# Kernel optimization log

Measured on AMD Instinct MI355X. Metric: run time of the kernel, lower is better.

The kernel has to match this reference:

```python
import jax, jax.numpy as jnp
import numpy as np

N = 50000
E = 800000
D = 128


def setup_inputs() -> dict:
    key = jax.random.key(0)
    ks = jax.random.split(key, 10)
    x = jax.random.normal(ks[0], (N, D), dtype=jnp.float32)
    edge_index = jax.random.randint(ks[1], (2, E), 0, N, dtype=jnp.int32)
    s = 1.0 / np.sqrt(D)
    W1 = jax.random.uniform(ks[2], (D, D), jnp.float32, -s, s)
    b1 = jnp.zeros((D,), jnp.float32)
    W2 = jax.random.uniform(ks[3], (D, D), jnp.float32, -s, s)
    b2 = jnp.zeros((D,), jnp.float32)
    Wt = jax.random.uniform(ks[4], (D, 1), jnp.float32, -s, s)
    bt = jnp.zeros((1,), jnp.float32)
    We = jax.random.uniform(ks[5], (D, 1), jnp.float32, -s, s)
    be = jnp.zeros((1,), jnp.float32)
    return {"x": x, "edge_index": edge_index, "W1": W1, "b1": b1,
            "W2": W2, "b2": b2, "Wt": Wt, "bt": bt, "We": We, "be": be}


def _gcn_norm(edge_index, n):
    # add self-loops, then symmetric normalization D^-1/2 (A+I) D^-1/2
    loop = jnp.arange(n, dtype=edge_index.dtype)
    src = jnp.concatenate([edge_index[0], loop])
    dst = jnp.concatenate([edge_index[1], loop])
    ones = jnp.ones(src.shape[0], dtype=jnp.float32)
    deg = jax.ops.segment_sum(ones, dst, num_segments=n)
    dinv = jnp.where(deg > 0, jax.lax.rsqrt(deg), 0.0)
    norm = dinv[src] * dinv[dst]  # [E+N]
    return src, dst, norm


def _gcn_conv(h, W, b, src, dst, norm, n):
    h = h @ W                                   # [N, D'] dense GEMM
    msg = h[src] * norm[:, None]                # gather + scale
    out = jax.ops.segment_sum(msg, dst, num_segments=n)  # scatter-add
    return out + b


def reference(x, edge_index, W1, b1, W2, b2, Wt, bt, We, be):
    n = x.shape[0]
    src, dst, norm = _gcn_norm(edge_index, n)
    h = jax.nn.relu(_gcn_conv(x, W1, b1, src, dst, norm, n))
    h = jax.nn.relu(_gcn_conv(h, W2, b2, src, dst, norm, n))
    # dropout is identity at inference (eval mode)
    survival_time = h @ Wt + bt   # [N, 1]
    event_status = h @ We + be    # [N, 1]
    return survival_time, event_status
```

## Files before the change

### kernel.cpp

```cpp
#include <hip/hip_runtime.h>
#include <hip/hip_fp16.h>
#include <math.h>

#define NN 50000
#define NE 800000
#define DD 128

#define NB  196
#define CAP 5300
#define EPB 4096

#define CONV_B 6250

#define SLAB (NN * 32)

typedef _Float16 half8_t __attribute__((ext_vector_type(8)));
typedef float f32x4 __attribute__((ext_vector_type(4)));


__global__ __launch_bounds__(256) void k_init_bcur(int* __restrict__ bcur) {
    int t = threadIdx.x;
    if (t < NB) bcur[t] = t * CAP;
}

__global__ __launch_bounds__(256) void k_phaseA(const int* __restrict__ src, const int* __restrict__ dst,
                                                int* __restrict__ bcur, unsigned int* __restrict__ ebuf) {
    __shared__ int hist[256];
    __shared__ int scanbuf[256];
    __shared__ int gbase[256];
    __shared__ unsigned int stage[EPB];
    __shared__ int tgt[EPB];

    const int tid = threadIdx.x;
    const int e0  = blockIdx.x * EPB;
    int nE = NE - e0; if (nE > EPB) nE = EPB;

    hist[tid] = 0;
    __syncthreads();

    unsigned int pk[16];
    unsigned int br[16];
    #pragma unroll
    for (int j = 0; j < 16; ++j) {
        int idx = tid + j * 256;
        if (idx < nE) {
            int e = e0 + idx;
            int s = src[e], d = dst[e];
            int b = d >> 8;
            int r = atomicAdd(&hist[b], 1);
            pk[j] = (unsigned int)s | ((unsigned int)(d & 255) << 16);
            br[j] = (unsigned int)b | ((unsigned int)r << 8);
        }
    }
    __syncthreads();
    int v = hist[tid];
    scanbuf[tid] = v;
    __syncthreads();
    for (int o = 1; o < 256; o <<= 1) {
        int t2 = (tid >= o) ? scanbuf[tid - o] : 0;
        __syncthreads();
        scanbuf[tid] += t2;
        __syncthreads();
    }
    int base_excl = scanbuf[tid] - v;
    if (tid < NB && v > 0) gbase[tid] = atomicAdd(&bcur[tid], v);
    hist[tid] = base_excl;
    __syncthreads();

    #pragma unroll
    for (int j = 0; j < 16; ++j) {
        int idx = tid + j * 256;
        if (idx < nE) {
            int b = br[j] & 255;
            int r = (int)(br[j] >> 8);
            int pos = hist[b] + r;
            stage[pos] = pk[j];
            tgt[pos]   = gbase[b] + r;
        }
    }
    __syncthreads();
    #pragma unroll
    for (int j = 0; j < 16; ++j) {
        int idx = tid + j * 256;
        if (idx < nE) ebuf[tgt[idx]] = stage[idx];
    }
}

__global__ __launch_bounds__(256) void k_build_csr(const unsigned int* __restrict__ ebuf,
                                                   const int* __restrict__ bcur,
                                                   int* __restrict__ row_ptr,
                                                   float* __restrict__ dinv,
                                                   unsigned short* __restrict__ col) {
    __shared__ int cnt[256];
    __shared__ int scanb[256];
    __shared__ unsigned short stage[CAP];

    const int b   = blockIdx.x;
    const int tid = threadIdx.x;
    const int seg0 = b * CAP;
    const int sb   = bcur[b] - seg0;
    const int n0   = b << 8;
    int nb = NN - n0; if (nb > 256) nb = 256;

    int sz_t = (tid < NB) ? (bcur[tid] - tid * CAP) : 0;
    scanb[tid] = sz_t;
    __syncthreads();
    for (int o = 1; o < 256; o <<= 1) {
        int t = (tid >= o) ? scanb[tid - o] : 0;
        __syncthreads();
        scanb[tid] += t;
        __syncthreads();
    }
    const int rbase = scanb[b] - sb;
    __syncthreads();

    cnt[tid] = 0;
    __syncthreads();
    for (int p = tid; p < sb; p += 256) {
        unsigned int e = ebuf[seg0 + p];
        atomicAdd(&cnt[(e >> 16) & 255], 1);
    }
    __syncthreads();
    int v = cnt[tid];
    scanb[tid] = v;
    __syncthreads();
    for (int o = 1; o < 256; o <<= 1) {
        int t = (tid >= o) ? scanb[tid - o] : 0;
        __syncthreads();
        scanb[tid] += t;
        __syncthreads();
    }
    int excl = scanb[tid] - v;
    if (tid < nb) {
        row_ptr[n0 + tid] = rbase + excl;
        dinv[n0 + tid] = rsqrtf(1.0f + (float)v);
    }
    if (b == 0 && tid == 0) row_ptr[NN] = NE;
    cnt[tid] = excl;
    __syncthreads();
    for (int p = tid; p < sb; p += 256) {
        unsigned int e = ebuf[seg0 + p];
        int pos = atomicAdd(&cnt[(e >> 16) & 255], 1);
        stage[pos] = (unsigned short)(e & 0xFFFFu);
    }
    __syncthreads();
    for (int p = tid; p < sb; p += 256) {
        col[rbase + p] = stage[p];
    }
}


__global__ __launch_bounds__(256) void k_prep(const float* __restrict__ x,
                                              const float* __restrict__ W1, const float* __restrict__ W2,
                                              __half* __restrict__ Xh,
                                              __half* __restrict__ WT1, __half* __restrict__ WT2) {
    int b = blockIdx.x;
    int tid = threadIdx.x;
    if (b < CONV_B) {
        int idx = b * 256 + tid;
        if (idx < (NN * DD) / 4) {
            float4 v = ((const float4*)x)[idx];
            __half2 a = __floats2half2_rn(v.x, v.y);
            __half2 c = __floats2half2_rn(v.z, v.w);
            uint2 pk;
            pk.x = *(unsigned int*)&a;
            pk.y = *(unsigned int*)&c;
            int row = idx >> 5;
            int c16 = idx & 31;
            int ch = c16 >> 3, wi = c16 & 7;
            *(uint2*)(Xh + (size_t)ch * SLAB + (size_t)row * 32 + wi * 4) = pk;
        }
    } else {
        const float* W  = (b == CONV_B) ? W1 : W2;
        __half*      WT = (b == CONV_B) ? WT1 : WT2;
        int n = tid >> 1;
        int k0 = (tid & 1) * 64;
        #pragma unroll 8
        for (int j = 0; j < 64; ++j) {
            int k = k0 + j;
            WT[n * DD + k] = __float2half(W[k * DD + n]);
        }
    }
}


#define LPAD 136

__global__ __launch_bounds__(256) void k_gemm_mfma(const __half* __restrict__ Xc, const __half* __restrict__ WT,
                                                   const float* __restrict__ dinv, __half* __restrict__ Gc) {
    __shared__ __half Wl[DD * LPAD];
    __shared__ __half Al[64 * LPAD];

    const int tid  = threadIdx.x;
    const int row0 = blockIdx.x * 64;

    {
        const uint4* WTg = (const uint4*)WT;
        #pragma unroll
        for (int j = 0; j < 8; ++j) {
            int u = tid + j * 256;
            int n = u >> 4, koff = (u & 15) * 8;
            uint4 v = WTg[u];
            *(uint4*)&Wl[n * LPAD + koff] = v;
        }
    }
    {
        #pragma unroll
        for (int j = 0; j < 4; ++j) {
            int u = tid + j * 256;
            int r = u >> 4, c16 = u & 15;
            int ch = c16 >> 2, wi = c16 & 3;
            int grow = row0 + r;
            uint4 v;
            if (grow < NN) v = *(const uint4*)(Xc + (size_t)ch * SLAB + (size_t)grow * 32 + wi * 8);
            else { v.x = 0; v.y = 0; v.z = 0; v.w = 0; }
            *(uint4*)&Al[r * LPAD + c16 * 8] = v;
        }
    }
    __syncthreads();

    const int wave = tid >> 6;
    const int lane = tid & 63;
    const int m    = lane & 15;
    const int quad = lane >> 4;

    f32x4 acc[8];
    #pragma unroll
    for (int t = 0; t < 8; ++t) acc[t] = (f32x4){0.f, 0.f, 0.f, 0.f};

    #pragma unroll
    for (int kk = 0; kk < DD; kk += 32) {
        half8_t a = *(const half8_t*)&Al[(wave * 16 + m) * LPAD + kk + quad * 8];
        #pragma unroll
        for (int t = 0; t < 8; ++t) {
            half8_t b = *(const half8_t*)&Wl[(t * 16 + m) * LPAD + kk + quad * 8];
            acc[t] = __builtin_amdgcn_mfma_f32_16x16x32_f16(a, b, acc[t], 0, 0, 0);
        }
    }

    __syncthreads();

    float4 dv = *(const float4*)&dinv[row0 + wave * 16 + quad * 4];

    #pragma unroll
    for (int t = 0; t < 8; ++t) {
        #pragma unroll
        for (int r = 0; r < 4; ++r) {
            int row_l = wave * 16 + quad * 4 + r;
            int c     = t * 16 + m;
            float val = acc[t][r] * ((const float*)&dv)[r];
            Al[row_l * LPAD + c] = __float2half(val);
        }
    }
    __syncthreads();

    {
        #pragma unroll
        for (int j = 0; j < 4; ++j) {
            int u = tid + j * 256;
            int r = u >> 4, c16 = u & 15;
            int ch = c16 >> 2, wi = c16 & 3;
            int grow = row0 + r;
            if (grow < NN) {
                uint4 v = *(const uint4*)&Al[r * LPAD + c16 * 8];
                *(uint4*)(Gc + (size_t)ch * SLAB + (size_t)grow * 32 + wi * 8) = v;
            }
        }
    }
}


__device__ inline float4 h4_to_f4(uint2 r) {
    __half2 a = *(__half2*)&r.x;
    __half2 b = *(__half2*)&r.y;
    float2 lo = __half22float2(a), hi = __half22float2(b);
    return make_float4(lo.x, lo.y, hi.x, hi.y);
}

__device__ inline uint2 f4_to_h4(float4 v) {
    __half2 a = __floats2half2_rn(v.x, v.y);
    __half2 b = __floats2half2_rn(v.z, v.w);
    uint2 r;
    r.x = *(unsigned int*)&a;
    r.y = *(unsigned int*)&b;
    return r;
}

__device__ inline float4 gather_grp(const __half* __restrict__ slab, int node, int fq,
                                    const unsigned short* __restrict__ col, int beg, int end) {
    float4 accA = h4_to_f4(*(const uint2*)(slab + (size_t)node * 32 + fq * 4));
    float4 accB = make_float4(0.f, 0.f, 0.f, 0.f);
    int p = beg;
    for (; p + 3 < end; p += 4) {
        int s0 = col[p], s1 = col[p + 1], s2 = col[p + 2], s3 = col[p + 3];
        float4 v0 = h4_to_f4(*(const uint2*)(slab + (size_t)s0 * 32 + fq * 4));
        float4 v1 = h4_to_f4(*(const uint2*)(slab + (size_t)s1 * 32 + fq * 4));
        float4 v2 = h4_to_f4(*(const uint2*)(slab + (size_t)s2 * 32 + fq * 4));
        float4 v3 = h4_to_f4(*(const uint2*)(slab + (size_t)s3 * 32 + fq * 4));
        accA.x += v0.x + v1.x; accA.y += v0.y + v1.y; accA.z += v0.z + v1.z; accA.w += v0.w + v1.w;
        accB.x += v2.x + v3.x; accB.y += v2.y + v3.y; accB.z += v2.z + v3.z; accB.w += v2.w + v3.w;
    }
    for (; p < end; ++p) {
        int s0 = col[p];
        float4 v0 = h4_to_f4(*(const uint2*)(slab + (size_t)s0 * 32 + fq * 4));
        accA.x += v0.x; accA.y += v0.y; accA.z += v0.z; accA.w += v0.w;
    }
    accA.x += accB.x; accA.y += accB.y; accA.z += accB.z; accA.w += accB.w;
    return accA;
}

__global__ __launch_bounds__(256) void k_aggregate_c(const __half* __restrict__ G, const float* __restrict__ dinv,
                                                     const int* __restrict__ row_ptr, const unsigned short* __restrict__ col,
                                                     const float* __restrict__ bias, __half* __restrict__ H) {
    const int bx    = blockIdx.x;
    const int slot  = bx & 7;
    const int chunk = slot >> 1;
    const int nb    = (bx >> 3) * 2 + (slot & 1);
    const int g     = threadIdx.x >> 3;
    const int fq    = threadIdx.x & 7;
    const int node  = nb * 32 + g;
    if (node >= NN) return;

    const __half* slab = G + (size_t)chunk * SLAB;
    int beg = row_ptr[node];
    int end = row_ptr[node + 1];
    float4 acc = gather_grp(slab, node, fq, col, beg, end);

    float di = dinv[node];
    float4 bv = *(const float4*)(bias + chunk * 32 + fq * 4);
    float4 hv;
    hv.x = fmaxf(fmaf(di, acc.x, bv.x), 0.f);
    hv.y = fmaxf(fmaf(di, acc.y, bv.y), 0.f);
    hv.z = fmaxf(fmaf(di, acc.z, bv.z), 0.f);
    hv.w = fmaxf(fmaf(di, acc.w, bv.w), 0.f);
    *(uint2*)(H + (size_t)chunk * SLAB + (size_t)node * 32 + fq * 4) = f4_to_h4(hv);
}

__global__ __launch_bounds__(256) void k_aggregate_heads_c(const __half* __restrict__ G, const float* __restrict__ dinv,
                                                           const int* __restrict__ row_ptr, const unsigned short* __restrict__ col,
                                                           const float* __restrict__ bias,
                                                           const float* __restrict__ Wt, const float* __restrict__ bt,
                                                           const float* __restrict__ We, const float* __restrict__ be,
                                                           float* __restrict__ out) {
    const int bx    = blockIdx.x;
    const int slot  = bx & 7;
    const int chunk = slot >> 1;
    const int nb    = (bx >> 3) * 2 + (slot & 1);
    const int g     = threadIdx.x >> 3;
    const int fq    = threadIdx.x & 7;
    const int node  = nb * 32 + g;
    if (node >= NN) return;

    const __half* slab = G + (size_t)chunk * SLAB;
    int beg = row_ptr[node];
    int end = row_ptr[node + 1];
    float4 acc = gather_grp(slab, node, fq, col, beg, end);

    float di = dinv[node];
    float4 bv = *(const float4*)(bias + chunk * 32 + fq * 4);
    float hx = fmaxf(fmaf(di, acc.x, bv.x), 0.f);
    float hy = fmaxf(fmaf(di, acc.y, bv.y), 0.f);
    float hz = fmaxf(fmaf(di, acc.z, bv.z), 0.f);
    float hw = fmaxf(fmaf(di, acc.w, bv.w), 0.f);

    float4 wt = *(const float4*)(Wt + chunk * 32 + fq * 4);
    float4 we = *(const float4*)(We + chunk * 32 + fq * 4);
    float t  = hx * wt.x + hy * wt.y + hz * wt.z + hw * wt.w;
    float ev = hx * we.x + hy * we.y + hz * we.z + hw * we.w;
    #pragma unroll
    for (int o = 1; o < 8; o <<= 1) {
        t  += __shfl_xor(t, o, 64);
        ev += __shfl_xor(ev, o, 64);
    }
    if (fq == 0) {
        if (chunk == 0) { t += bt[0]; ev += be[0]; }
        atomicAdd(&out[node], t);
        atomicAdd(&out[NN + node], ev);
    }
}


extern "C" void kernel_launch(void* const* d_in, const int* in_sizes, int n_in,
                              void* d_out, int out_size, void* d_ws, size_t ws_size,
                              hipStream_t stream) {
    const float* x  = (const float*)d_in[0];
    const int*   ei = (const int*)d_in[1];
    const float* W1 = (const float*)d_in[2];
    const float* b1 = (const float*)d_in[3];
    const float* W2 = (const float*)d_in[4];
    const float* b2 = (const float*)d_in[5];
    const float* Wt = (const float*)d_in[6];
    const float* bt = (const float*)d_in[7];
    const float* We = (const float*)d_in[8];
    const float* be = (const float*)d_in[9];
    float* out = (float*)d_out;

    const int* srcI = ei;
    const int* dstI = ei + NE;

    char* w = (char*)d_ws;
    __half*         Xh    = (__half*)w;         w += (size_t)NN * DD * sizeof(__half);
    __half*         Gh    = (__half*)w;         w += (size_t)NN * DD * sizeof(__half);
    __half*         H1h   = (__half*)w;         w += (size_t)NN * DD * sizeof(__half);
    __half*         WT1   = (__half*)w;         w += (size_t)DD * DD * sizeof(__half);
    __half*         WT2   = (__half*)w;         w += (size_t)DD * DD * sizeof(__half);
    unsigned int*   ebuf  = (unsigned int*)w;   w += (size_t)NB * CAP * sizeof(unsigned int);
    unsigned short* col   = (unsigned short*)w; w += (size_t)NE * sizeof(unsigned short);
    float*          dinv  = (float*)w;          w += (size_t)(NN + 64) * sizeof(float);
    int*            rowp  = (int*)w;            w += (size_t)(NN + 1) * sizeof(int);
    int*            bcur  = (int*)w;            w += (size_t)NB * sizeof(int);

    const int A_B    = (NE + EPB - 1) / EPB;
    const int NBLK   = (NN + 31) / 32;
    const int AGG_B  = ((NBLK + 1) / 2) * 8;
    const int GEMM_B = (NN + 63) / 64;

    hipMemsetAsync(out, 0, (size_t)out_size * sizeof(float), stream);

    hipLaunchKernelGGL(k_init_bcur,  dim3(1),          dim3(256), 0, stream, bcur);
    hipLaunchKernelGGL(k_phaseA,     dim3(A_B),        dim3(256), 0, stream, srcI, dstI, bcur, ebuf);
    hipLaunchKernelGGL(k_build_csr,  dim3(NB),         dim3(256), 0, stream, ebuf, bcur, rowp, dinv, col);
    hipLaunchKernelGGL(k_prep,       dim3(CONV_B + 2), dim3(256), 0, stream, x, W1, W2, Xh, WT1, WT2);

    hipLaunchKernelGGL(k_gemm_mfma,   dim3(GEMM_B), dim3(256), 0, stream, Xh, WT1, dinv, Gh);
    hipLaunchKernelGGL(k_aggregate_c, dim3(AGG_B),  dim3(256), 0, stream, Gh, dinv, rowp, col, b1, H1h);

    hipLaunchKernelGGL(k_gemm_mfma,         dim3(GEMM_B), dim3(256), 0, stream, H1h, WT2, dinv, Gh);
    hipLaunchKernelGGL(k_aggregate_heads_c, dim3(AGG_B),  dim3(256), 0, stream, Gh, dinv, rowp, col, b2,
                       Wt, bt, We, be, out);
}
```

Measured before the change: 211.0 us.

## Widen feature slabs to 64 channels and merge edge bucketing with conversion prep

The fp16 feature matrices now use two 64-wide column slabs instead of four 32-wide ones. Each aggregation thread group covers 16 lanes of 64 features, so each gathered neighbour row segment is 128 bytes and there are half as many chunk passes over the edge lists. The edge-bucketing phase, the x/W fp16 conversion and the weight transpose are fused into one launch, and a memset replaces the bucket-cursor init kernel. This removes two launches, but the gather footprint per pass grows, which may reduce L2 locality per slab.

```diff
diff --git a/kernel.cpp b/kernel.cpp
--- a/kernel.cpp
+++ b/kernel.cpp
@@ -9,155 +9,86 @@
 #define NB  196
 #define CAP 5300
 #define EPB 4096
+#define A_BLOCKS 196
 
 #define CONV_B 6250
 
-#define SLAB (NN * 32)
+#define SLAB2 (NN * 64)
 
 typedef _Float16 half8_t __attribute__((ext_vector_type(8)));
 typedef float f32x4 __attribute__((ext_vector_type(4)));
 
 
-__global__ __launch_bounds__(256) void k_init_bcur(int* __restrict__ bcur) {
-    int t = threadIdx.x;
-    if (t < NB) bcur[t] = t * CAP;
-}
-
-__global__ __launch_bounds__(256) void k_phaseA(const int* __restrict__ src, const int* __restrict__ dst,
-                                                int* __restrict__ bcur, unsigned int* __restrict__ ebuf) {
-    __shared__ int hist[256];
-    __shared__ int scanbuf[256];
-    __shared__ int gbase[256];
-    __shared__ unsigned int stage[EPB];
-    __shared__ int tgt[EPB];
-
+__global__ __launch_bounds__(256) void k_setup(const int* __restrict__ src, const int* __restrict__ dst,
+                                               int* __restrict__ bcnt, unsigned int* __restrict__ ebuf,
+                                               const float* __restrict__ x,
+                                               const float* __restrict__ W1, const float* __restrict__ W2,
+                                               __half* __restrict__ Xh,
+                                               __half* __restrict__ WT1, __half* __restrict__ WT2) {
+    const int blk = blockIdx.x;
     const int tid = threadIdx.x;
-    const int e0  = blockIdx.x * EPB;
-    int nE = NE - e0; if (nE > EPB) nE = EPB;
-
-    hist[tid] = 0;
-    __syncthreads();
-
-    unsigned int pk[16];
-    unsigned int br[16];
-    #pragma unroll
-    for (int j = 0; j < 16; ++j) {
-        int idx = tid + j * 256;
-        if (idx < nE) {
-            int e = e0 + idx;
-            int s = src[e], d = dst[e];
-            int b = d >> 8;
-            int r = atomicAdd(&hist[b], 1);
-            pk[j] = (unsigned int)s | ((unsigned int)(d & 255) << 16);
-            br[j] = (unsigned int)b | ((unsigned int)r << 8);
-        }
-    }
-    __syncthreads();
-    int v = hist[tid];
-    scanbuf[tid] = v;
-    __syncthreads();
-    for (int o = 1; o < 256; o <<= 1) {
-        int t2 = (tid >= o) ? scanbuf[tid - o] : 0;
-        __syncthreads();
-        scanbuf[tid] += t2;
-        __syncthreads();
-    }
-    int base_excl = scanbuf[tid] - v;
-    if (tid < NB && v > 0) gbase[tid] = atomicAdd(&bcur[tid], v);
-    hist[tid] = base_excl;
-    __syncthreads();
-
-    #pragma unroll
-    for (int j = 0; j < 16; ++j) {
-        int idx = tid + j * 256;
-        if (idx < nE) {
-            int b = br[j] & 255;
-            int r = (int)(br[j] >> 8);
-            int pos = hist[b] + r;
-            stage[pos] = pk[j];
-            tgt[pos]   = gbase[b] + r;
-        }
-    }
-    __syncthreads();
-    #pragma unroll
-    for (int j = 0; j < 16; ++j) {
-        int idx = tid + j * 256;
-        if (idx < nE) ebuf[tgt[idx]] = stage[idx];
-    }
-}
-
-__global__ __launch_bounds__(256) void k_build_csr(const unsigned int* __restrict__ ebuf,
-                                                   const int* __restrict__ bcur,
-                                                   int* __restrict__ row_ptr,
-                                                   float* __restrict__ dinv,
-                                                   unsigned short* __restrict__ col) {
-    __shared__ int cnt[256];
-    __shared__ int scanb[256];
-    __shared__ unsigned short stage[CAP];
-
-    const int b   = blockIdx.x;
-    const int tid = threadIdx.x;
-    const int seg0 = b * CAP;
-    const int sb   = bcur[b] - seg0;
-    const int n0   = b << 8;
-    int nb = NN - n0; if (nb > 256) nb = 256;
-
-    int sz_t = (tid < NB) ? (bcur[tid] - tid * CAP) : 0;
-    scanb[tid] = sz_t;
-    __syncthreads();
-    for (int o = 1; o < 256; o <<= 1) {
-        int t = (tid >= o) ? scanb[tid - o] : 0;
-        __syncthreads();
-        scanb[tid] += t;
-        __syncthreads();
-    }
-    const int rbase = scanb[b] - sb;
-    __syncthreads();
-
-    cnt[tid] = 0;
-    __syncthreads();
-    for (int p = tid; p < sb; p += 256) {
-        unsigned int e = ebuf[seg0 + p];
-        atomicAdd(&cnt[(e >> 16) & 255], 1);
-    }
-    __syncthreads();
-    int v = cnt[tid];
-    scanb[tid] = v;
-    __syncthreads();
-    for (int o = 1; o < 256; o <<= 1) {
-        int t = (tid >= o) ? scanb[tid - o] : 0;
-        __syncthreads();
-        scanb[tid] += t;
-        __syncthreads();
-    }
-    int excl = scanb[tid] - v;
-    if (tid < nb) {
-        row_ptr[n0 + tid] = rbase + excl;
-        dinv[n0 + tid] = rsqrtf(1.0f + (float)v);
-    }
-    if (b == 0 && tid == 0) row_ptr[NN] = NE;
-    cnt[tid] = excl;
-    __syncthreads();
-    for (int p = tid; p < sb; p += 256) {
-        unsigned int e = ebuf[seg0 + p];
-        int pos = atomicAdd(&cnt[(e >> 16) & 255], 1);
-        stage[pos] = (unsigned short)(e & 0xFFFFu);
-    }
-    __syncthreads();
-    for (int p = tid; p < sb; p += 256) {
-        col[rbase + p] = stage[p];
-    }
-}
-
-
-__global__ __launch_bounds__(256) void k_prep(const float* __restrict__ x,
-                                              const float* __restrict__ W1, const float* __restrict__ W2,
-                                              __half* __restrict__ Xh,
-                                              __half* __restrict__ WT1, __half* __restrict__ WT2) {
-    int b = blockIdx.x;
-    int tid = threadIdx.x;
-    if (b < CONV_B) {
-        int idx = b * 256 + tid;
+
+    if (blk < A_BLOCKS) {
+        __shared__ int hist[256];
+        __shared__ int scanbuf[256];
+        __shared__ int gbase[256];
+        __shared__ unsigned int stage[EPB];
+        __shared__ int tgt[EPB];
+
+        const int e0 = blk * EPB;
+        int nE = NE - e0; if (nE > EPB) nE = EPB;
+
+        hist[tid] = 0;
+        __syncthreads();
+
+        unsigned int pk[16];
+        unsigned int br[16];
+        #pragma unroll
+        for (int j = 0; j < 16; ++j) {
+            int idx = tid + j * 256;
+            if (idx < nE) {
+                int e = e0 + idx;
+                int s = src[e], d = dst[e];
+                int b = d >> 8;
+                int r = atomicAdd(&hist[b], 1);
+                pk[j] = (unsigned int)s | ((unsigned int)(d & 255) << 16);
+                br[j] = (unsigned int)b | ((unsigned int)r << 8);
+            }
+        }
+        __syncthreads();
+        int v = hist[tid];
+        scanbuf[tid] = v;
+        __syncthreads();
+        for (int o = 1; o < 256; o <<= 1) {
+            int t2 = (tid >= o) ? scanbuf[tid - o] : 0;
+            __syncthreads();
+            scanbuf[tid] += t2;
+            __syncthreads();
+        }
+        int base_excl = scanbuf[tid] - v;
+        if (tid < NB && v > 0) gbase[tid] = tid * CAP + atomicAdd(&bcnt[tid], v);
+        hist[tid] = base_excl;
+        __syncthreads();
+
+        #pragma unroll
+        for (int j = 0; j < 16; ++j) {
+            int idx = tid + j * 256;
+            if (idx < nE) {
+                int b = br[j] & 255;
+                int r = (int)(br[j] >> 8);
+                int pos = hist[b] + r;
+                stage[pos] = pk[j];
+                tgt[pos]   = gbase[b] + r;
+            }
+        }
+        __syncthreads();
+        #pragma unroll
+        for (int j = 0; j < 16; ++j) {
+            int idx = tid + j * 256;
+            if (idx < nE) ebuf[tgt[idx]] = stage[idx];
+        }
+    } else if (blk < A_BLOCKS + CONV_B) {
+        int idx = (blk - A_BLOCKS) * 256 + tid;
         if (idx < (NN * DD) / 4) {
             float4 v = ((const float4*)x)[idx];
             __half2 a = __floats2half2_rn(v.x, v.y);
@@ -167,12 +98,12 @@
             pk.y = *(unsigned int*)&c;
             int row = idx >> 5;
             int c16 = idx & 31;
-            int ch = c16 >> 3, wi = c16 & 7;
-            *(uint2*)(Xh + (size_t)ch * SLAB + (size_t)row * 32 + wi * 4) = pk;
+            int ch = c16 >> 4, wi = c16 & 15;
+            *(uint2*)(Xh + (size_t)ch * SLAB2 + (size_t)row * 64 + wi * 4) = pk;
         }
     } else {
-        const float* W  = (b == CONV_B) ? W1 : W2;
-        __half*      WT = (b == CONV_B) ? WT1 : WT2;
+        const float* W  = (blk == A_BLOCKS + CONV_B) ? W1 : W2;
+        __half*      WT = (blk == A_BLOCKS + CONV_B) ? WT1 : WT2;
         int n = tid >> 1;
         int k0 = (tid & 1) * 64;
         #pragma unroll 8
@@ -184,6 +115,70 @@
 }
 
 
+__global__ __launch_bounds__(256) void k_build_csr(const unsigned int* __restrict__ ebuf,
+                                                   const int* __restrict__ bcnt,
+                                                   int* __restrict__ row_ptr,
+                                                   float* __restrict__ dinv,
+                                                   unsigned short* __restrict__ col) {
+    __shared__ int cnt[256];
+    __shared__ int scanb[256];
+    __shared__ unsigned short stage[CAP];
+
+    const int b   = blockIdx.x;
+    const int tid = threadIdx.x;
+    const int seg0 = b * CAP;
+    const int sb   = bcnt[b];
+    const int n0   = b << 8;
+    int nb = NN - n0; if (nb > 256) nb = 256;
+
+    int sz_t = (tid < NB) ? bcnt[tid] : 0;
+    scanb[tid] = sz_t;
+    __syncthreads();
+    for (int o = 1; o < 256; o <<= 1) {
+        int t = (tid >= o) ? scanb[tid - o] : 0;
+        __syncthreads();
+        scanb[tid] += t;
+        __syncthreads();
+    }
+    const int rbase = scanb[b] - sb;
+    __syncthreads();
+
+    cnt[tid] = 0;
+    __syncthreads();
+    for (int p = tid; p < sb; p += 256) {
+        unsigned int e = ebuf[seg0 + p];
+        atomicAdd(&cnt[(e >> 16) & 255], 1);
+    }
+    __syncthreads();
+    int v = cnt[tid];
+    scanb[tid] = v;
+    __syncthreads();
+    for (int o = 1; o < 256; o <<= 1) {
+        int t = (tid >= o) ? scanb[tid - o] : 0;
+        __syncthreads();
+        scanb[tid] += t;
+        __syncthreads();
+    }
+    int excl = scanb[tid] - v;
+    if (tid < nb) {
+        row_ptr[n0 + tid] = rbase + excl;
+        dinv[n0 + tid] = rsqrtf(1.0f + (float)v);
+    }
+    if (b == 0 && tid == 0) row_ptr[NN] = NE;
+    cnt[tid] = excl;
+    __syncthreads();
+    for (int p = tid; p < sb; p += 256) {
+        unsigned int e = ebuf[seg0 + p];
+        int pos = atomicAdd(&cnt[(e >> 16) & 255], 1);
+        stage[pos] = (unsigned short)(e & 0xFFFFu);
+    }
+    __syncthreads();
+    for (int p = tid; p < sb; p += 256) {
+        col[rbase + p] = stage[p];
+    }
+}
+
+
 #define LPAD 136
 
 __global__ __launch_bounds__(256) void k_gemm_mfma(const __half* __restrict__ Xc, const __half* __restrict__ WT,
@@ -209,10 +204,10 @@
         for (int j = 0; j < 4; ++j) {
             int u = tid + j * 256;
             int r = u >> 4, c16 = u & 15;
-            int ch = c16 >> 2, wi = c16 & 3;
+            int ch = c16 >> 3, wi = c16 & 7;
             int grow = row0 + r;
             uint4 v;
-            if (grow < NN) v = *(const uint4*)(Xc + (size_t)ch * SLAB + (size_t)grow * 32 + wi * 8);
+            if (grow < NN) v = *(const uint4*)(Xc + (size_t)ch * SLAB2 + (size_t)grow * 64 + wi * 8);
             else { v.x = 0; v.y = 0; v.z = 0; v.w = 0; }
             *(uint4*)&Al[r * LPAD + c16 * 8] = v;
         }
@@ -259,11 +254,11 @@
         for (int j = 0; j < 4; ++j) {
             int u = tid + j * 256;
             int r = u >> 4, c16 = u & 15;
-            int ch = c16 >> 2, wi = c16 & 3;
+            int ch = c16 >> 3, wi = c16 & 7;
             int grow = row0 + r;
             if (grow < NN) {
                 uint4 v = *(const uint4*)&Al[r * LPAD + c16 * 8];
-                *(uint4*)(Gc + (size_t)ch * SLAB + (size_t)grow * 32 + wi * 8) = v;
+                *(uint4*)(Gc + (size_t)ch * SLAB2 + (size_t)grow * 64 + wi * 8) = v;
             }
         }
     }
@@ -286,23 +281,24 @@
     return r;
 }
 
-__device__ inline float4 gather_grp(const __half* __restrict__ slab, int node, int fq,
-                                    const unsigned short* __restrict__ col, int beg, int end) {
-    float4 accA = h4_to_f4(*(const uint2*)(slab + (size_t)node * 32 + fq * 4));
+__device__ inline float4 gather_grp64(const __half* __restrict__ slab, int node, int fl,
+                                      const unsigned short* __restrict__ col, int beg, int end) {
+    const __half* base = slab + fl * 4;
+    float4 accA = h4_to_f4(*(const uint2*)(base + (size_t)node * 64));
     float4 accB = make_float4(0.f, 0.f, 0.f, 0.f);
     int p = beg;
     for (; p + 3 < end; p += 4) {
         int s0 = col[p], s1 = col[p + 1], s2 = col[p + 2], s3 = col[p + 3];
-        float4 v0 = h4_to_f4(*(const uint2*)(slab + (size_t)s0 * 32 + fq * 4));
-        float4 v1 = h4_to_f4(*(const uint2*)(slab + (size_t)s1 * 32 + fq * 4));
-        float4 v2 = h4_to_f4(*(const uint2*)(slab + (size_t)s2 * 32 + fq * 4));
-        float4 v3 = h4_to_f4(*(const uint2*)(slab + (size_t)s3 * 32 + fq * 4));
+        float4 v0 = h4_to_f4(*(const uint2*)(base + (size_t)s0 * 64));
+        float4 v1 = h4_to_f4(*(const uint2*)(base + (size_t)s1 * 64));
+        float4 v2 = h4_to_f4(*(const uint2*)(base + (size_t)s2 * 64));
+        float4 v3 = h4_to_f4(*(const uint2*)(base + (size_t)s3 * 64));
         accA.x += v0.x + v1.x; accA.y += v0.y + v1.y; accA.z += v0.z + v1.z; accA.w += v0.w + v1.w;
         accB.x += v2.x + v3.x; accB.y += v2.y + v3.y; accB.z += v2.z + v3.z; accB.w += v2.w + v3.w;
     }
     for (; p < end; ++p) {
         int s0 = col[p];
-        float4 v0 = h4_to_f4(*(const uint2*)(slab + (size_t)s0 * 32 + fq * 4));
+        float4 v0 = h4_to_f4(*(const uint2*)(base + (size_t)s0 * 64));
         accA.x += v0.x; accA.y += v0.y; accA.z += v0.z; accA.w += v0.w;
     }
     accA.x += accB.x; accA.y += accB.y; accA.z += accB.z; accA.w += accB.w;
@@ -314,26 +310,26 @@
                                                      const float* __restrict__ bias, __half* __restrict__ H) {
     const int bx    = blockIdx.x;
     const int slot  = bx & 7;
-    const int chunk = slot >> 1;
-    const int nb    = (bx >> 3) * 2 + (slot & 1);
-    const int g     = threadIdx.x >> 3;
-    const int fq    = threadIdx.x & 7;
-    const int node  = nb * 32 + g;
+    const int chunk = slot >> 2;
+    const int nb    = (bx >> 3) * 4 + (slot & 3);
+    const int g     = threadIdx.x >> 4;
+    const int fl    = threadIdx.x & 15;
+    const int node  = nb * 16 + g;
     if (node >= NN) return;
 
-    const __half* slab = G + (size_t)chunk * SLAB;
+    const __half* slab = G + (size_t)chunk * SLAB2;
     int beg = row_ptr[node];
     int end = row_ptr[node + 1];
-    float4 acc = gather_grp(slab, node, fq, col, beg, end);
+    float4 acc = gather_grp64(slab, node, fl, col, beg, end);
 
     float di = dinv[node];
-    float4 bv = *(const float4*)(bias + chunk * 32 + fq * 4);
+    float4 bv = *(const float4*)(bias + chunk * 64 + fl * 4);
     float4 hv;
     hv.x = fmaxf(fmaf(di, acc.x, bv.x), 0.f);
     hv.y = fmaxf(fmaf(di, acc.y, bv.y), 0.f);
     hv.z = fmaxf(fmaf(di, acc.z, bv.z), 0.f);
     hv.w = fmaxf(fmaf(di, acc.w, bv.w), 0.f);
-    *(uint2*)(H + (size_t)chunk * SLAB + (size_t)node * 32 + fq * 4) = f4_to_h4(hv);
+    *(uint2*)(H + (size_t)chunk * SLAB2 + (size_t)node * 64 + fl * 4) = f4_to_h4(hv);
 }
 
 __global__ __launch_bounds__(256) void k_aggregate_heads_c(const __half* __restrict__ G, const float* __restrict__ dinv,
@@ -344,35 +340,35 @@
                                                            float* __restrict__ out) {
     const int bx    = blockIdx.x;
     const int slot  = bx & 7;
-    const int chunk = slot >> 1;
-    const int nb    = (bx >> 3) * 2 + (slot & 1);
-    const int g     = threadIdx.x >> 3;
-    const int fq    = threadIdx.x & 7;
-    const int node  = nb * 32 + g;
+    const int chunk = slot >> 2;
+    const int nb    = (bx >> 3) * 4 + (slot & 3);
+    const int g     = threadIdx.x >> 4;
+    const int fl    = threadIdx.x & 15;
+    const int node  = nb * 16 + g;
     if (node >= NN) return;
 
-    const __half* slab = G + (size_t)chunk * SLAB;
+    const __half* slab = G + (size_t)chunk * SLAB2;
     int beg = row_ptr[node];
     int end = row_ptr[node + 1];
-    float4 acc = gather_grp(slab, node, fq, col, beg, end);
+    float4 acc = gather_grp64(slab, node, fl, col, beg, end);
 
     float di = dinv[node];
-    float4 bv = *(const float4*)(bias + chunk * 32 + fq * 4);
+    float4 bv = *(const float4*)(bias + chunk * 64 + fl * 4);
     float hx = fmaxf(fmaf(di, acc.x, bv.x), 0.f);
     float hy = fmaxf(fmaf(di, acc.y, bv.y), 0.f);
     float hz = fmaxf(fmaf(di, acc.z, bv.z), 0.f);
     float hw = fmaxf(fmaf(di, acc.w, bv.w), 0.f);
 
-    float4 wt = *(const float4*)(Wt + chunk * 32 + fq * 4);
-    float4 we = *(const float4*)(We + chunk * 32 + fq * 4);
+    float4 wt = *(const float4*)(Wt + chunk * 64 + fl * 4);
+    float4 we = *(const float4*)(We + chunk * 64 + fl * 4);
     float t  = hx * wt.x + hy * wt.y + hz * wt.z + hw * wt.w;
     float ev = hx * we.x + hy * we.y + hz * we.z + hw * we.w;
     #pragma unroll
-    for (int o = 1; o < 8; o <<= 1) {
+    for (int o = 1; o < 16; o <<= 1) {
         t  += __shfl_xor(t, o, 64);
         ev += __shfl_xor(ev, o, 64);
     }
-    if (fq == 0) {
+    if (fl == 0) {
         if (chunk == 0) { t += bt[0]; ev += be[0]; }
         atomicAdd(&out[node], t);
         atomicAdd(&out[NN + node], ev);
@@ -408,19 +404,19 @@
     unsigned short* col   = (unsigned short*)w; w += (size_t)NE * sizeof(unsigned short);
     float*          dinv  = (float*)w;          w += (size_t)(NN + 64) * sizeof(float);
     int*            rowp  = (int*)w;            w += (size_t)(NN + 1) * sizeof(int);
-    int*            bcur  = (int*)w;            w += (size_t)NB * sizeof(int);
-
-    const int A_B    = (NE + EPB - 1) / EPB;
-    const int NBLK   = (NN + 31) / 32;
-    const int AGG_B  = ((NBLK + 1) / 2) * 8;
-    const int GEMM_B = (NN + 63) / 64;
+    int*            bcnt  = (int*)w;            w += (size_t)NB * sizeof(int);
+
+    const int SETUP_B = A_BLOCKS + CONV_B + 2;
+    const int NBLK    = (NN + 15) / 16;
+    const int AGG_B   = ((NBLK + 3) / 4) * 8;
+    const int GEMM_B  = (NN + 63) / 64;
 
     hipMemsetAsync(out, 0, (size_t)out_size * sizeof(float), stream);
-
-    hipLaunchKernelGGL(k_init_bcur,  dim3(1),          dim3(256), 0, stream, bcur);
-    hipLaunchKernelGGL(k_phaseA,     dim3(A_B),        dim3(256), 0, stream, srcI, dstI, bcur, ebuf);
-    hipLaunchKernelGGL(k_build_csr,  dim3(NB),         dim3(256), 0, stream, ebuf, bcur, rowp, dinv, col);
-    hipLaunchKernelGGL(k_prep,       dim3(CONV_B + 2), dim3(256), 0, stream, x, W1, W2, Xh, WT1, WT2);
+    hipMemsetAsync(bcnt, 0, (size_t)NB * sizeof(int), stream);
+
+    hipLaunchKernelGGL(k_setup,     dim3(SETUP_B), dim3(256), 0, stream,
+                       srcI, dstI, bcnt, ebuf, x, W1, W2, Xh, WT1, WT2);
+    hipLaunchKernelGGL(k_build_csr, dim3(NB),      dim3(256), 0, stream, ebuf, bcnt, rowp, dinv, col);
 
     hipLaunchKernelGGL(k_gemm_mfma,   dim3(GEMM_B), dim3(256), 0, stream, Xh, WT1, dinv, Gh);
     hipLaunchKernelGGL(k_aggregate_c, dim3(AGG_B),  dim3(256), 0, stream, Gh, dinv, rowp, col, b1, H1h);
```

Result: no change. 209.1 us (-0.9%).
